# Optimization experiments

Hardware: AMD Instinct MI355X
Metric: run time of the kernel (lower is better)

## Reference

```python
import jax, jax.numpy as jnp
import numpy as np

N, E, F_IN, H, O = 50000, 800000, 128, 64, 1


def _gcn_conv(x, row, col, ew, W, b, n_nodes):
    """PyG GCNConv: add self-loops (weight 1), symmetric deg normalization,
    linear transform (no bias inside lin), scatter-add aggregation, then +bias."""
    loop = jnp.arange(n_nodes, dtype=row.dtype)
    r = jnp.concatenate([row, loop])
    c = jnp.concatenate([col, loop])
    w = jnp.concatenate([ew, jnp.ones((n_nodes,), dtype=ew.dtype)])
    deg = jax.ops.segment_sum(w, c, num_segments=n_nodes)            # [N]
    dis = jnp.where(deg > 0, jax.lax.rsqrt(jnp.maximum(deg, 1e-12)), 0.0)
    norm = dis[r] * w * dis[c]                                       # [E+N]
    h = x @ W                                                        # [N, out]
    msg = h[r] * norm[:, None]                                       # gather + scale
    agg = jax.ops.segment_sum(msg, c, num_segments=n_nodes)          # scatter-add
    return agg + b


def setup_inputs() -> dict:
    key = jax.random.key(0)
    ks = jax.random.split(key, 14)
    s = 0.02
    return {
        "x": jax.random.normal(ks[0], (N, F_IN), dtype=jnp.float32),
        "edge_index": jax.random.randint(ks[1], (2, E), 0, N, dtype=jnp.int64),
        "edge_weight": jax.random.uniform(ks[2], (E,), dtype=jnp.float32),
        "W1": jax.random.normal(ks[3], (F_IN, H), dtype=jnp.float32) * s,
        "b1": jnp.zeros((H,), dtype=jnp.float32),
        "W2": jax.random.normal(ks[4], (H, H), dtype=jnp.float32) * s,
        "b2": jnp.zeros((H,), dtype=jnp.float32),
        "W_ih": jax.random.normal(ks[5], (4 * H, H), dtype=jnp.float32) * s,
        "W_hh": jax.random.normal(ks[6], (4 * H, H), dtype=jnp.float32) * s,
        "b_ih": jax.random.normal(ks[7], (4 * H,), dtype=jnp.float32) * s,
        "b_hh": jax.random.normal(ks[8], (4 * H,), dtype=jnp.float32) * s,
        "W_reg": jax.random.normal(ks[9], (H, O), dtype=jnp.float32) * s,
        "b_reg": jnp.zeros((O,), dtype=jnp.float32),
    }


def reference(x, edge_index, edge_weight, W1, b1, W2, b2,
              W_ih, W_hh, b_ih, b_hh, W_reg, b_reg):
    row, col = edge_index[0], edge_index[1]
    n = x.shape[0]
    h = jax.nn.relu(_gcn_conv(x, row, col, edge_weight, W1, b1, n))
    h = jax.nn.relu(_gcn_conv(h, row, col, edge_weight, W2, b2, n))
    # single-step LSTM, zero initial (h0, c0); PyTorch gate order i, f, g, o
    hd = W_ih.shape[1]
    h0 = jnp.zeros((n, hd), dtype=h.dtype)
    gates = h @ W_ih.T + h0 @ W_hh.T + b_ih + b_hh                   # [N, 4H]
    i, f, g, o = jnp.split(gates, 4, axis=-1)
    c = jax.nn.sigmoid(f) * 0.0 + jax.nn.sigmoid(i) * jnp.tanh(g)    # c0 = 0
    hn = jax.nn.sigmoid(o) * jnp.tanh(c)                             # lstm_out[:, -1]
    return hn @ W_reg + b_reg
```

## Files before the change

### kernel.cpp

```cpp
#include <hip/hip_runtime.h>
#include <math.h>


#define QN 12544
#define NPAD (4 * QN)
#define NSLICE 64

__device__ __forceinline__ float sigmoidf_(float x) {
    return 1.0f / (1.0f + expf(-x));
}

__global__ __launch_bounds__(256) void hist_k(const int* __restrict__ col,
                                              int* __restrict__ part, int E, int N) {
    __shared__ int hloc[QN];
    const int t = threadIdx.x;
    const int s = blockIdx.x >> 2;
    const int q = blockIdx.x & 3;
    const int lo = q * QN;
    for (int i = t; i < QN; i += 256) hloc[i] = 0;
    __syncthreads();
    const int per = (E + NSLICE - 1) / NSLICE;
    const int e0 = s * per, e1 = min(E, e0 + per);
    for (int e = e0 + t; e < e1; e += 256) {
        int c = col[e];
        unsigned rel = (unsigned)(c - lo);
        if (rel < (unsigned)QN && (unsigned)c < (unsigned)N)
            atomicAdd(&hloc[rel], 1);
    }
    __syncthreads();
    int* dst = part + (size_t)s * NPAD + lo;
    for (int i = t; i < QN; i += 256) dst[i] = hloc[i];
}

__global__ __launch_bounds__(256) void hreduce_k(const int* __restrict__ part,
                                                 int* __restrict__ cnt) {
    int i = blockIdx.x * 256 + threadIdx.x;
    if (i >= NPAD) return;
    const int* p = part + i;
    int s0 = 0, s1 = 0, s2 = 0, s3 = 0;
    for (int s = 0; s < NSLICE; s += 4) {
        s0 += p[(size_t)(s + 0) * NPAD];
        s1 += p[(size_t)(s + 1) * NPAD];
        s2 += p[(size_t)(s + 2) * NPAD];
        s3 += p[(size_t)(s + 3) * NPAD];
    }
    cnt[i] = (s0 + s1) + (s2 + s3);
}

__global__ __launch_bounds__(256) void scanA_k(const int* __restrict__ cnt,
                                               int* __restrict__ bsum, int N) {
    __shared__ int r[256];
    int t = threadIdx.x, i = blockIdx.x * 256 + t;
    r[t] = (i < N) ? cnt[i] : 0;
    __syncthreads();
#pragma unroll
    for (int off = 128; off > 0; off >>= 1) {
        if (t < off) r[t] += r[t + off];
        __syncthreads();
    }
    if (t == 0) bsum[blockIdx.x] = r[0];
}

__global__ __launch_bounds__(256) void scanB_k(int* __restrict__ bsum,
                                               int* __restrict__ rowptr, int NB, int N) {
    __shared__ int s[2][256];
    int t = threadIdx.x;
    int v = (t < NB) ? bsum[t] : 0;
    int pin = 0;
    s[0][t] = v;
    __syncthreads();
#pragma unroll
    for (int off = 1; off < 256; off <<= 1) {
        int x = s[pin][t];
        if (t >= off) x += s[pin][t - off];
        s[pin ^ 1][t] = x;
        pin ^= 1;
        __syncthreads();
    }
    int incl = s[pin][t];
    if (t < NB) bsum[t] = incl - v;
    if (t == 255) rowptr[N] = incl;
}

__global__ __launch_bounds__(256) void scanC_k(const int* __restrict__ cnt,
                                               const int* __restrict__ bsum,
                                               int* __restrict__ rowptr,
                                               int* __restrict__ cursor, int N) {
    __shared__ int s[2][256];
    int t = threadIdx.x, i = blockIdx.x * 256 + t;
    int v = (i < N) ? cnt[i] : 0;
    int pin = 0;
    s[0][t] = v;
    __syncthreads();
#pragma unroll
    for (int off = 1; off < 256; off <<= 1) {
        int x = s[pin][t];
        if (t >= off) x += s[pin][t - off];
        s[pin ^ 1][t] = x;
        pin ^= 1;
        __syncthreads();
    }
    int excl = s[pin][t] - v + bsum[blockIdx.x];
    if (i < N) { rowptr[i] = excl; cursor[i] = excl; }
}

__global__ __launch_bounds__(256) void fill_k(const int* __restrict__ row,
                                              const int* __restrict__ col,
                                              const float* __restrict__ ew,
                                              int* __restrict__ cursor,
                                              int2* __restrict__ pairs, int E, int N) {
    int e = blockIdx.x * 256 + threadIdx.x;
    if (e >= E) return;
    int r = row[e], c = col[e];
    if ((unsigned)c >= (unsigned)N) return;
    float w = ew[e];
    if ((unsigned)r >= (unsigned)N) { r = 0; w = 0.0f; }
    int pos = __hip_atomic_fetch_add(&cursor[c], 1, __ATOMIC_RELAXED, __HIP_MEMORY_SCOPE_AGENT);
    pairs[pos] = make_int2(r, __float_as_int(w));
}

__global__ __launch_bounds__(256) void degsum_k(const int* __restrict__ rowptr,
                                                const int2* __restrict__ pairs,
                                                float* __restrict__ dis, int N) {
    int i = blockIdx.x * 256 + threadIdx.x;
    if (i >= N) return;
    int b = rowptr[i], en = rowptr[i + 1];
    float s = 0.0f;
    for (int e = b; e < en; ++e) s += __int_as_float(pairs[e].y);
    dis[i] = rsqrtf(s + 1.0f);
}

__global__ __launch_bounds__(256) void scale_k(int2* __restrict__ pairs,
                                               const float* __restrict__ dis, int E) {
    int e = blockIdx.x * 256 + threadIdx.x;
    if (e >= E) return;
    int2 p = pairs[e];
    p.y = __float_as_int(__int_as_float(p.y) * dis[p.x]);
    pairs[e] = p;
}

__global__ __launch_bounds__(256) void aggregate_k(const float* __restrict__ h,
                                                   const int* __restrict__ rowptr,
                                                   const int2* __restrict__ pairs,
                                                   const float* __restrict__ dis,
                                                   const float* __restrict__ b,
                                                   float* __restrict__ out, int N) {
    const int t = threadIdx.x;
    const int lane = t & 63;
    const int node = blockIdx.x * 4 + (t >> 6);
    if (node >= N) return;

    const int beg = rowptr[node], end = rowptr[node + 1];
    float acc = 0.0f;
    for (int base = beg; base < end; base += 64) {
        int n = min(64, end - base);
        int src = 0; float val = 0.0f;
        if (lane < n) {
            int2 p = pairs[base + lane];
            src = p.x; val = __int_as_float(p.y);
        }
        int j = 0;
        for (; j + 4 <= n; j += 4) {
            int   s0 = __shfl(src, j),     s1 = __shfl(src, j + 1);
            int   s2 = __shfl(src, j + 2), s3 = __shfl(src, j + 3);
            float v0 = __shfl(val, j),     v1 = __shfl(val, j + 1);
            float v2 = __shfl(val, j + 2), v3 = __shfl(val, j + 3);
            float h0 = h[(size_t)s0 * 64 + lane];
            float h1 = h[(size_t)s1 * 64 + lane];
            float h2 = h[(size_t)s2 * 64 + lane];
            float h3 = h[(size_t)s3 * 64 + lane];
            acc = fmaf(h0, v0, acc);
            acc = fmaf(h1, v1, acc);
            acc = fmaf(h2, v2, acc);
            acc = fmaf(h3, v3, acc);
        }
        for (; j < n; ++j) {
            int s0 = __shfl(src, j);
            float v0 = __shfl(val, j);
            acc = fmaf(h[(size_t)s0 * 64 + lane], v0, acc);
        }
    }
    float d = dis[node];
    acc = fmaf(d, h[(size_t)node * 64 + lane], acc);
    acc = fmaf(d, acc, b[lane]);
    out[(size_t)node * 64 + lane] = fmaxf(acc, 0.0f);
}

template <int K>
__global__ __launch_bounds__(256) void gemm64_k(const float* __restrict__ A,
                                                const float* __restrict__ W,
                                                float* __restrict__ C, int M) {
    __shared__ float xs[64][68];
    __shared__ float ws[K][64];
    const int t  = threadIdx.x;
    const int n0 = blockIdx.x * 64;

    for (int base = t * 4; base < K * 64; base += 1024)
        *(float4*)((float*)ws + base) = *(const float4*)(W + base);

    const int cg = t & 15, ng = t >> 4;
    const int col = cg * 4, nb = ng * 4;
    float acc[4][4];
#pragma unroll
    for (int i = 0; i < 4; ++i)
#pragma unroll
        for (int j = 0; j < 4; ++j) acc[i][j] = 0.0f;

    for (int k0 = 0; k0 < K; k0 += 64) {
        __syncthreads();
        for (int base = t * 4; base < 64 * 64; base += 1024) {
            int r = base >> 6, k = base & 63;
            int node = n0 + r;
            float4 v = make_float4(0.f, 0.f, 0.f, 0.f);
            if (node < M) v = *(const float4*)(A + (size_t)node * K + k0 + k);
            *(float4*)&xs[r][k] = v;
        }
        __syncthreads();
#pragma unroll 4
        for (int kk = 0; kk < 64; kk += 4) {
            float4 a[4];
#pragma unroll
            for (int i = 0; i < 4; ++i) a[i] = *(float4*)&xs[nb + i][kk];
#pragma unroll
            for (int j = 0; j < 4; ++j) {
                float4 bv = *(float4*)&ws[k0 + kk + j][col];
                float av[4];
                switch (j) {
                    case 0: av[0]=a[0].x; av[1]=a[1].x; av[2]=a[2].x; av[3]=a[3].x; break;
                    case 1: av[0]=a[0].y; av[1]=a[1].y; av[2]=a[2].y; av[3]=a[3].y; break;
                    case 2: av[0]=a[0].z; av[1]=a[1].z; av[2]=a[2].z; av[3]=a[3].z; break;
                    default:av[0]=a[0].w; av[1]=a[1].w; av[2]=a[2].w; av[3]=a[3].w; break;
                }
#pragma unroll
                for (int i = 0; i < 4; ++i) {
                    acc[i][0] = fmaf(av[i], bv.x, acc[i][0]);
                    acc[i][1] = fmaf(av[i], bv.y, acc[i][1]);
                    acc[i][2] = fmaf(av[i], bv.z, acc[i][2]);
                    acc[i][3] = fmaf(av[i], bv.w, acc[i][3]);
                }
            }
        }
    }
#pragma unroll
    for (int i = 0; i < 4; ++i) {
        int node = n0 + nb + i;
        if (node < M)
            *(float4*)(C + (size_t)node * 64 + col) =
                make_float4(acc[i][0], acc[i][1], acc[i][2], acc[i][3]);
    }
}

__global__ __launch_bounds__(256) void lstm_head_k(const float* __restrict__ h,
                                                   const float* __restrict__ Wih,
                                                   const float* __restrict__ bih,
                                                   const float* __restrict__ bhh,
                                                   const float* __restrict__ Wreg,
                                                   const float* __restrict__ breg,
                                                   float* __restrict__ out, int N) {
    __shared__ float wt[64 * 192];
    __shared__ float hsT[64 * 64];
    const int t = threadIdx.x;
    const int n0 = blockIdx.x * 64;

    {
        const int j = t & 63, kq = (t >> 6) * 4;
#pragma unroll
        for (int gid = 0; gid < 3; ++gid) {
            const int gBase = (gid == 0) ? 0 : (gid == 1 ? 128 : 192);
            const int gOff = gid * 64;
#pragma unroll
            for (int it = 0; it < 4; ++it) {
                int k0 = it * 16 + kq;
                float4 w = *(const float4*)(Wih + (size_t)(gBase + j) * 64 + k0);
                wt[(k0 + 0) * 192 + gOff + j] = w.x;
                wt[(k0 + 1) * 192 + gOff + j] = w.y;
                wt[(k0 + 2) * 192 + gOff + j] = w.z;
                wt[(k0 + 3) * 192 + gOff + j] = w.w;
            }
        }
    }
    {
        const int r = t & 63, kq = (t >> 6) * 4;
        const int node = n0 + r;
#pragma unroll
        for (int it = 0; it < 4; ++it) {
            int k0 = it * 16 + kq;
            float4 v = make_float4(0.f, 0.f, 0.f, 0.f);
            if (node < N) v = *(const float4*)(h + (size_t)node * 64 + k0);
            hsT[(k0 + 0) * 64 + r] = v.x;
            hsT[(k0 + 1) * 64 + r] = v.y;
            hsT[(k0 + 2) * 64 + r] = v.z;
            hsT[(k0 + 3) * 64 + r] = v.w;
        }
    }

    const int cg = t & 15, ng = t >> 4;
    const int col = cg * 4, nb = ng * 4;
    float4 bi4 = *(const float4*)(bih + col);
    float4 bg4 = *(const float4*)(bih + 128 + col);
    float4 bo4 = *(const float4*)(bih + 192 + col);
    {
        float4 h0 = *(const float4*)(bhh + col);
        float4 h1 = *(const float4*)(bhh + 128 + col);
        float4 h2 = *(const float4*)(bhh + 192 + col);
        bi4.x += h0.x; bi4.y += h0.y; bi4.z += h0.z; bi4.w += h0.w;
        bg4.x += h1.x; bg4.y += h1.y; bg4.z += h1.z; bg4.w += h1.w;
        bo4.x += h2.x; bo4.y += h2.y; bo4.z += h2.z; bo4.w += h2.w;
    }
    float4 wr4 = *(const float4*)(Wreg + col);
    const float br = breg[0];

    __syncthreads();

    float ai[4][4], ag[4][4], ao[4][4];
#pragma unroll
    for (int i = 0; i < 4; ++i)
#pragma unroll
        for (int j = 0; j < 4; ++j) { ai[i][j] = 0.f; ag[i][j] = 0.f; ao[i][j] = 0.f; }

#pragma unroll 4
    for (int k = 0; k < 64; ++k) {
        float4 a  = *(float4*)&hsT[k * 64 + nb];
        float4 wi = *(float4*)&wt[k * 192 + col];
        float4 wg = *(float4*)&wt[k * 192 + 64 + col];
        float4 wo = *(float4*)&wt[k * 192 + 128 + col];
        const float av[4] = {a.x, a.y, a.z, a.w};
#pragma unroll
        for (int i = 0; i < 4; ++i) {
            ai[i][0] = fmaf(av[i], wi.x, ai[i][0]);
            ai[i][1] = fmaf(av[i], wi.y, ai[i][1]);
            ai[i][2] = fmaf(av[i], wi.z, ai[i][2]);
            ai[i][3] = fmaf(av[i], wi.w, ai[i][3]);
            ag[i][0] = fmaf(av[i], wg.x, ag[i][0]);
            ag[i][1] = fmaf(av[i], wg.y, ag[i][1]);
            ag[i][2] = fmaf(av[i], wg.z, ag[i][2]);
            ag[i][3] = fmaf(av[i], wg.w, ag[i][3]);
            ao[i][0] = fmaf(av[i], wo.x, ao[i][0]);
            ao[i][1] = fmaf(av[i], wo.y, ao[i][1]);
            ao[i][2] = fmaf(av[i], wo.z, ao[i][2]);
            ao[i][3] = fmaf(av[i], wo.w, ao[i][3]);
        }
    }

    const float bia[4] = {bi4.x, bi4.y, bi4.z, bi4.w};
    const float bga[4] = {bg4.x, bg4.y, bg4.z, bg4.w};
    const float boa[4] = {bo4.x, bo4.y, bo4.z, bo4.w};
    const float wra[4] = {wr4.x, wr4.y, wr4.z, wr4.w};
    float res[4];
#pragma unroll
    for (int i = 0; i < 4; ++i) {
        float s = 0.f;
#pragma unroll
        for (int j = 0; j < 4; ++j) {
            float gi = ai[i][j] + bia[j];
            float gg = ag[i][j] + bga[j];
            float go = ao[i][j] + boa[j];
            float cc = sigmoidf_(gi) * tanhf(gg);
            float hn = sigmoidf_(go) * tanhf(cc);
            s = fmaf(hn, wra[j], s);
        }
        res[i] = s;
    }
#pragma unroll
    for (int off = 8; off > 0; off >>= 1) {
#pragma unroll
        for (int i = 0; i < 4; ++i) res[i] += __shfl_down(res[i], off);
    }
    if (cg == 0) {
#pragma unroll
        for (int i = 0; i < 4; ++i) {
            int node = n0 + nb + i;
            if (node < N) out[node] = res[i] + br;
        }
    }
}

extern "C" void kernel_launch(void* const* d_in, const int* in_sizes, int n_in,
                              void* d_out, int out_size, void* d_ws, size_t ws_size,
                              hipStream_t stream) {
    const float* x    = (const float*)d_in[0];
    const int*   ei   = (const int*)d_in[1];
    const float* ew   = (const float*)d_in[2];
    const float* W1   = (const float*)d_in[3];
    const float* b1   = (const float*)d_in[4];
    const float* W2   = (const float*)d_in[5];
    const float* b2   = (const float*)d_in[6];
    const float* Wih  = (const float*)d_in[7];
    const float* bih  = (const float*)d_in[9];
    const float* bhh  = (const float*)d_in[10];
    const float* Wreg = (const float*)d_in[11];
    const float* breg = (const float*)d_in[12];
    float* out = (float*)d_out;

    const int N = out_size;
    const int E = in_sizes[1] / 2;
    const int* row = ei;
    const int* col = ei + E;

    const int NB = (N + 255) / 256;

    char* wsb = (char*)d_ws;
    size_t off = 0;
    int*   part   = (int*)  (wsb + off);
    float* bufA   = (float*)(wsb + off); off += (size_t)NSLICE * NPAD * 4;
    int2*  pairs  = (int2*) (wsb + off); off += (size_t)E * 8;
    float* dis    = (float*)(wsb + off); off += (size_t)NPAD * 4;
    int*   cnt    = (int*)  (wsb + off); off += (size_t)NPAD * 4;
    int*   rowptr = (int*)  (wsb + off); off += ((size_t)NPAD + 64) * 4;
    int*   cursor = (int*)  (wsb + off); off += (size_t)NPAD * 4;
    int*   bsum   = (int*)  (wsb + off); off += 1024;
    float* bufB   = (float*)(wsb + off); off += (size_t)N * 64 * 4;
    float* bufC   = (float*)(wsb + off); off += (size_t)N * 64 * 4;

    const int eb = (E + 255) / 256;
    const int gb = (N + 63) / 64;
    const int ab = (N + 3) / 4;

    hist_k<<<NSLICE * 4, 256, 0, stream>>>(col, part, E, N);
    hreduce_k<<<NPAD / 256, 256, 0, stream>>>(part, cnt);
    scanA_k<<<NB, 256, 0, stream>>>(cnt, bsum, N);
    scanB_k<<<1, 256, 0, stream>>>(bsum, rowptr, NB, N);
    scanC_k<<<NB, 256, 0, stream>>>(cnt, bsum, rowptr, cursor, N);
    fill_k<<<eb, 256, 0, stream>>>(row, col, ew, cursor, pairs, E, N);
    degsum_k<<<NB, 256, 0, stream>>>(rowptr, pairs, dis, N);
    scale_k<<<eb, 256, 0, stream>>>(pairs, dis, E);

    gemm64_k<128><<<gb, 256, 0, stream>>>(x, W1, bufA, N);
    aggregate_k<<<ab, 256, 0, stream>>>(bufA, rowptr, pairs, dis, b1, bufB, N);

    gemm64_k<64><<<gb, 256, 0, stream>>>(bufB, W2, bufC, N);
    aggregate_k<<<ab, 256, 0, stream>>>(bufC, rowptr, pairs, dis, b2, bufA, N);

    lstm_head_k<<<gb, 256, 0, stream>>>(bufA, Wih, bih, bhh, Wreg, breg, out, N);
}
```

Baseline: 313.8 us.

## Compute degree in histogram and fill CSR via per-slice LDS cursors with full norm

The histogram pass now also accumulates edge weights per slice, so the per-slice prefix kernel produces slice offsets, counts and inverse-sqrt degrees together. Filling then uses per-slice shared-memory cursors instead of global atomics, and stores the fully normalized weight (w*dis[r]*dis[c]). This removes the separate degree-sum and scale kernels and the contended global atomics. In exchange it adds a second float histogram in LDS (doubling shared memory per block and lowering occupancy), writes the slice offset array, and has fill re-scan all edges over 256 blocks. The aggregate epilogue is adjusted to apply the self-loop term as d*d.

```diff
diff --git a/kernel.cpp b/kernel.cpp
--- a/kernel.cpp
+++ b/kernel.cpp
@@ -11,40 +11,48 @@
 }
 
 __global__ __launch_bounds__(256) void hist_k(const int* __restrict__ col,
-                                              int* __restrict__ part, int E, int N) {
-    __shared__ int hloc[QN];
+                                              const float* __restrict__ ew,
+                                              int* __restrict__ part_i,
+                                              float* __restrict__ part_f, int E, int N) {
+    __shared__ int   hc[QN];
+    __shared__ float hw[QN];
     const int t = threadIdx.x;
     const int s = blockIdx.x >> 2;
     const int q = blockIdx.x & 3;
     const int lo = q * QN;
-    for (int i = t; i < QN; i += 256) hloc[i] = 0;
+    for (int i = t; i < QN; i += 256) { hc[i] = 0; hw[i] = 0.0f; }
     __syncthreads();
     const int per = (E + NSLICE - 1) / NSLICE;
     const int e0 = s * per, e1 = min(E, e0 + per);
     for (int e = e0 + t; e < e1; e += 256) {
         int c = col[e];
         unsigned rel = (unsigned)(c - lo);
-        if (rel < (unsigned)QN && (unsigned)c < (unsigned)N)
-            atomicAdd(&hloc[rel], 1);
-    }
-    __syncthreads();
-    int* dst = part + (size_t)s * NPAD + lo;
-    for (int i = t; i < QN; i += 256) dst[i] = hloc[i];
-}
-
-__global__ __launch_bounds__(256) void hreduce_k(const int* __restrict__ part,
-                                                 int* __restrict__ cnt) {
+        if (rel < (unsigned)QN && (unsigned)c < (unsigned)N) {
+            atomicAdd(&hc[rel], 1);
+            atomicAdd(&hw[rel], ew[e]);
+        }
+    }
+    __syncthreads();
+    int*   di = part_i + (size_t)s * NPAD + lo;
+    float* df = part_f + (size_t)s * NPAD + lo;
+    for (int i = t; i < QN; i += 256) { di[i] = hc[i]; df[i] = hw[i]; }
+}
+
+__global__ __launch_bounds__(256) void prefix_k(const int* __restrict__ part_i,
+                                                const float* __restrict__ part_f,
+                                                int* __restrict__ coff,
+                                                int* __restrict__ cnt,
+                                                float* __restrict__ dis) {
     int i = blockIdx.x * 256 + threadIdx.x;
-    if (i >= NPAD) return;
-    const int* p = part + i;
-    int s0 = 0, s1 = 0, s2 = 0, s3 = 0;
-    for (int s = 0; s < NSLICE; s += 4) {
-        s0 += p[(size_t)(s + 0) * NPAD];
-        s1 += p[(size_t)(s + 1) * NPAD];
-        s2 += p[(size_t)(s + 2) * NPAD];
-        s3 += p[(size_t)(s + 3) * NPAD];
-    }
-    cnt[i] = (s0 + s1) + (s2 + s3);
+    int acc = 0; float wacc = 0.0f;
+    for (int s = 0; s < NSLICE; ++s) {
+        size_t idx = (size_t)s * NPAD + i;
+        coff[idx] = acc;
+        acc  += part_i[idx];
+        wacc += part_f[idx];
+    }
+    cnt[i] = acc;
+    dis[i] = rsqrtf(wacc + 1.0f);
 }
 
 __global__ __launch_bounds__(256) void scanA_k(const int* __restrict__ cnt,
@@ -84,8 +92,7 @@
 
 __global__ __launch_bounds__(256) void scanC_k(const int* __restrict__ cnt,
                                                const int* __restrict__ bsum,
-                                               int* __restrict__ rowptr,
-                                               int* __restrict__ cursor, int N) {
+                                               int* __restrict__ rowptr, int N) {
     __shared__ int s[2][256];
     int t = threadIdx.x, i = blockIdx.x * 256 + t;
     int v = (i < N) ? cnt[i] : 0;
@@ -101,42 +108,39 @@
         __syncthreads();
     }
     int excl = s[pin][t] - v + bsum[blockIdx.x];
-    if (i < N) { rowptr[i] = excl; cursor[i] = excl; }
+    if (i < N) rowptr[i] = excl;
 }
 
 __global__ __launch_bounds__(256) void fill_k(const int* __restrict__ row,
                                               const int* __restrict__ col,
                                               const float* __restrict__ ew,
-                                              int* __restrict__ cursor,
+                                              const int* __restrict__ rowptr,
+                                              const int* __restrict__ coff,
+                                              const float* __restrict__ dis,
                                               int2* __restrict__ pairs, int E, int N) {
-    int e = blockIdx.x * 256 + threadIdx.x;
-    if (e >= E) return;
-    int r = row[e], c = col[e];
-    if ((unsigned)c >= (unsigned)N) return;
-    float w = ew[e];
-    if ((unsigned)r >= (unsigned)N) { r = 0; w = 0.0f; }
-    int pos = __hip_atomic_fetch_add(&cursor[c], 1, __ATOMIC_RELAXED, __HIP_MEMORY_SCOPE_AGENT);
-    pairs[pos] = make_int2(r, __float_as_int(w));
-}
-
-__global__ __launch_bounds__(256) void degsum_k(const int* __restrict__ rowptr,
-                                                const int2* __restrict__ pairs,
-                                                float* __restrict__ dis, int N) {
-    int i = blockIdx.x * 256 + threadIdx.x;
-    if (i >= N) return;
-    int b = rowptr[i], en = rowptr[i + 1];
-    float s = 0.0f;
-    for (int e = b; e < en; ++e) s += __int_as_float(pairs[e].y);
-    dis[i] = rsqrtf(s + 1.0f);
-}
-
-__global__ __launch_bounds__(256) void scale_k(int2* __restrict__ pairs,
-                                               const float* __restrict__ dis, int E) {
-    int e = blockIdx.x * 256 + threadIdx.x;
-    if (e >= E) return;
-    int2 p = pairs[e];
-    p.y = __float_as_int(__int_as_float(p.y) * dis[p.x]);
-    pairs[e] = p;
+    __shared__ int lcur[QN];
+    const int t = threadIdx.x;
+    const int s = blockIdx.x >> 2;
+    const int q = blockIdx.x & 3;
+    const int lo = q * QN;
+    const int* cof = coff + (size_t)s * NPAD + lo;
+    const int* rp  = rowptr + lo;
+    for (int i = t; i < QN; i += 256) lcur[i] = rp[i] + cof[i];
+    __syncthreads();
+    const int per = (E + NSLICE - 1) / NSLICE;
+    const int e0 = s * per, e1 = min(E, e0 + per);
+    for (int e = e0 + t; e < e1; e += 256) {
+        int c = col[e];
+        unsigned rel = (unsigned)(c - lo);
+        if (rel < (unsigned)QN && (unsigned)c < (unsigned)N) {
+            int r = row[e];
+            float w = ew[e];
+            if ((unsigned)r >= (unsigned)N) { r = 0; w = 0.0f; }
+            float nv = w * dis[r] * dis[c];
+            int pos = atomicAdd(&lcur[rel], 1);
+            pairs[pos] = make_int2(r, __float_as_int(nv));
+        }
+    }
 }
 
 __global__ __launch_bounds__(256) void aggregate_k(const float* __restrict__ h,
@@ -181,8 +185,7 @@
         }
     }
     float d = dis[node];
-    acc = fmaf(d, h[(size_t)node * 64 + lane], acc);
-    acc = fmaf(d, acc, b[lane]);
+    acc = fmaf(d * d, h[(size_t)node * 64 + lane], acc) + b[lane];
     out[(size_t)node * 64 + lane] = fmaxf(acc, 0.0f);
 }
 
@@ -399,31 +402,31 @@
 
     const int NB = (N + 255) / 256;
 
+    const size_t REG = ((size_t)NSLICE * NPAD > (size_t)N * 64 ? (size_t)NSLICE * NPAD
+                                                               : (size_t)N * 64) * 4;
     char* wsb = (char*)d_ws;
     size_t off = 0;
-    int*   part   = (int*)  (wsb + off);
-    float* bufA   = (float*)(wsb + off); off += (size_t)NSLICE * NPAD * 4;
+    int*   part_i = (int*)  (wsb + off);
+    float* bufA   = (float*)(wsb + off); off += REG;
+    float* part_f = (float*)(wsb + off);
+    float* bufB   = (float*)(wsb + off); off += REG;
+    int*   coff   = (int*)  (wsb + off);
+    float* bufC   = (float*)(wsb + off); off += REG;
     int2*  pairs  = (int2*) (wsb + off); off += (size_t)E * 8;
     float* dis    = (float*)(wsb + off); off += (size_t)NPAD * 4;
     int*   cnt    = (int*)  (wsb + off); off += (size_t)NPAD * 4;
     int*   rowptr = (int*)  (wsb + off); off += ((size_t)NPAD + 64) * 4;
-    int*   cursor = (int*)  (wsb + off); off += (size_t)NPAD * 4;
     int*   bsum   = (int*)  (wsb + off); off += 1024;
-    float* bufB   = (float*)(wsb + off); off += (size_t)N * 64 * 4;
-    float* bufC   = (float*)(wsb + off); off += (size_t)N * 64 * 4;
-
-    const int eb = (E + 255) / 256;
+
     const int gb = (N + 63) / 64;
     const int ab = (N + 3) / 4;
 
-    hist_k<<<NSLICE * 4, 256, 0, stream>>>(col, part, E, N);
-    hreduce_k<<<NPAD / 256, 256, 0, stream>>>(part, cnt);
+    hist_k<<<NSLICE * 4, 256, 0, stream>>>(col, ew, part_i, part_f, E, N);
+    prefix_k<<<NPAD / 256, 256, 0, stream>>>(part_i, part_f, coff, cnt, dis);
     scanA_k<<<NB, 256, 0, stream>>>(cnt, bsum, N);
     scanB_k<<<1, 256, 0, stream>>>(bsum, rowptr, NB, N);
-    scanC_k<<<NB, 256, 0, stream>>>(cnt, bsum, rowptr, cursor, N);
-    fill_k<<<eb, 256, 0, stream>>>(row, col, ew, cursor, pairs, E, N);
-    degsum_k<<<NB, 256, 0, stream>>>(rowptr, pairs, dis, N);
-    scale_k<<<eb, 256, 0, stream>>>(pairs, dis, E);
+    scanC_k<<<NB, 256, 0, stream>>>(cnt, bsum, rowptr, N);
+    fill_k<<<NSLICE * 4, 256, 0, stream>>>(row, col, ew, rowptr, coff, dis, pairs, E, N);
 
     gemm64_k<128><<<gb, 256, 0, stream>>>(x, W1, bufA, N);
     aggregate_k<<<ab, 256, 0, stream>>>(bufA, rowptr, pairs, dis, b1, bufB, N);
```

After: 311.2 us. Within noise of the previous version (-0.8%).

## Replace global-atomic CSR fill with slice-local LDS cursors; aggregate two nodes per wave

Applied to the files above, without the earlier changes.

Histogram now uses 128 edge slices times 8 node octants with 16-bit per-slice counts. A prefix kernel turns these into per-slice offsets, so the fill kernel can place edges using LDS atomics on per-slice cursors instead of global atomics on a cursor array. The aggregate kernel processes two destination nodes per wavefront so more gathers are in flight at once. Workspace regions are overlapped to fit the new 16-bit buffers. The 16-bit counts would overflow if one slice put more than 65535 edges on a single node, and each fill block rescans its whole edge slice for every octant.

```diff
diff --git a/kernel.cpp b/kernel.cpp
--- a/kernel.cpp
+++ b/kernel.cpp
@@ -2,49 +2,58 @@
 #include <math.h>
 
 
-#define QN 12544
-#define NPAD (4 * QN)
-#define NSLICE 64
+#define QN 6272
+#define NOCT 8
+#define NPAD (NOCT * QN)
+#define NSLICE 128
 
 __device__ __forceinline__ float sigmoidf_(float x) {
     return 1.0f / (1.0f + expf(-x));
 }
 
 __global__ __launch_bounds__(256) void hist_k(const int* __restrict__ col,
-                                              int* __restrict__ part, int E, int N) {
-    __shared__ int hloc[QN];
+                                              unsigned short* __restrict__ part,
+                                              int E, int N) {
+    __shared__ int hc[QN];
     const int t = threadIdx.x;
-    const int s = blockIdx.x >> 2;
-    const int q = blockIdx.x & 3;
+    const int s = blockIdx.x >> 3;
+    const int q = blockIdx.x & 7;
     const int lo = q * QN;
-    for (int i = t; i < QN; i += 256) hloc[i] = 0;
+    for (int i = t; i < QN; i += 256) hc[i] = 0;
     __syncthreads();
     const int per = (E + NSLICE - 1) / NSLICE;
     const int e0 = s * per, e1 = min(E, e0 + per);
-    for (int e = e0 + t; e < e1; e += 256) {
+    int e = e0 + t;
+    for (; e + 768 < e1; e += 1024) {
+        int c0 = col[e], c1 = col[e + 256], c2 = col[e + 512], c3 = col[e + 768];
+        unsigned r0 = (unsigned)(c0 - lo), r1 = (unsigned)(c1 - lo);
+        unsigned r2 = (unsigned)(c2 - lo), r3 = (unsigned)(c3 - lo);
+        if (r0 < (unsigned)QN && (unsigned)c0 < (unsigned)N) atomicAdd(&hc[r0], 1);
+        if (r1 < (unsigned)QN && (unsigned)c1 < (unsigned)N) atomicAdd(&hc[r1], 1);
+        if (r2 < (unsigned)QN && (unsigned)c2 < (unsigned)N) atomicAdd(&hc[r2], 1);
+        if (r3 < (unsigned)QN && (unsigned)c3 < (unsigned)N) atomicAdd(&hc[r3], 1);
+    }
+    for (; e < e1; e += 256) {
         int c = col[e];
         unsigned rel = (unsigned)(c - lo);
-        if (rel < (unsigned)QN && (unsigned)c < (unsigned)N)
-            atomicAdd(&hloc[rel], 1);
-    }
-    __syncthreads();
-    int* dst = part + (size_t)s * NPAD + lo;
-    for (int i = t; i < QN; i += 256) dst[i] = hloc[i];
-}
-
-__global__ __launch_bounds__(256) void hreduce_k(const int* __restrict__ part,
-                                                 int* __restrict__ cnt) {
+        if (rel < (unsigned)QN && (unsigned)c < (unsigned)N) atomicAdd(&hc[rel], 1);
+    }
+    __syncthreads();
+    unsigned short* dst = part + (size_t)s * NPAD + lo;
+    for (int i = t; i < QN; i += 256) dst[i] = (unsigned short)hc[i];
+}
+
+__global__ __launch_bounds__(256) void prefix_k(const unsigned short* __restrict__ part,
+                                                unsigned short* __restrict__ coff,
+                                                int* __restrict__ cnt) {
     int i = blockIdx.x * 256 + threadIdx.x;
-    if (i >= NPAD) return;
-    const int* p = part + i;
-    int s0 = 0, s1 = 0, s2 = 0, s3 = 0;
-    for (int s = 0; s < NSLICE; s += 4) {
-        s0 += p[(size_t)(s + 0) * NPAD];
-        s1 += p[(size_t)(s + 1) * NPAD];
-        s2 += p[(size_t)(s + 2) * NPAD];
-        s3 += p[(size_t)(s + 3) * NPAD];
-    }
-    cnt[i] = (s0 + s1) + (s2 + s3);
+    int acc = 0;
+    for (int s = 0; s < NSLICE; ++s) {
+        size_t idx = (size_t)s * NPAD + i;
+        coff[idx] = (unsigned short)acc;
+        acc += part[idx];
+    }
+    cnt[i] = acc;
 }
 
 __global__ __launch_bounds__(256) void scanA_k(const int* __restrict__ cnt,
@@ -84,8 +93,7 @@
 
 __global__ __launch_bounds__(256) void scanC_k(const int* __restrict__ cnt,
                                                const int* __restrict__ bsum,
-                                               int* __restrict__ rowptr,
-                                               int* __restrict__ cursor, int N) {
+                                               int* __restrict__ rowptr, int N) {
     __shared__ int s[2][256];
     int t = threadIdx.x, i = blockIdx.x * 256 + t;
     int v = (i < N) ? cnt[i] : 0;
@@ -101,22 +109,61 @@
         __syncthreads();
     }
     int excl = s[pin][t] - v + bsum[blockIdx.x];
-    if (i < N) { rowptr[i] = excl; cursor[i] = excl; }
+    if (i < N) rowptr[i] = excl;
 }
 
 __global__ __launch_bounds__(256) void fill_k(const int* __restrict__ row,
                                               const int* __restrict__ col,
                                               const float* __restrict__ ew,
-                                              int* __restrict__ cursor,
+                                              const int* __restrict__ rowptr,
+                                              const unsigned short* __restrict__ coff,
                                               int2* __restrict__ pairs, int E, int N) {
-    int e = blockIdx.x * 256 + threadIdx.x;
-    if (e >= E) return;
-    int r = row[e], c = col[e];
-    if ((unsigned)c >= (unsigned)N) return;
-    float w = ew[e];
-    if ((unsigned)r >= (unsigned)N) { r = 0; w = 0.0f; }
-    int pos = __hip_atomic_fetch_add(&cursor[c], 1, __ATOMIC_RELAXED, __HIP_MEMORY_SCOPE_AGENT);
-    pairs[pos] = make_int2(r, __float_as_int(w));
+    __shared__ int lcur[QN];
+    const int t = threadIdx.x;
+    const int s = blockIdx.x >> 3;
+    const int q = blockIdx.x & 7;
+    const int lo = q * QN;
+    const unsigned short* cof = coff + (size_t)s * NPAD + lo;
+    const int* rp = rowptr + lo;
+    for (int i = t; i < QN; i += 256) lcur[i] = rp[i] + (int)cof[i];
+    __syncthreads();
+    const int per = (E + NSLICE - 1) / NSLICE;
+    const int e0 = s * per, e1 = min(E, e0 + per);
+    int e = e0 + t;
+    for (; e + 768 < e1; e += 1024) {
+        int c0 = col[e], c1 = col[e + 256], c2 = col[e + 512], c3 = col[e + 768];
+        unsigned r0 = (unsigned)(c0 - lo), r1 = (unsigned)(c1 - lo);
+        unsigned r2 = (unsigned)(c2 - lo), r3 = (unsigned)(c3 - lo);
+        if (r0 < (unsigned)QN && (unsigned)c0 < (unsigned)N) {
+            int r = row[e]; float w = ew[e];
+            if ((unsigned)r >= (unsigned)N) { r = 0; w = 0.0f; }
+            pairs[atomicAdd(&lcur[r0], 1)] = make_int2(r, __float_as_int(w));
+        }
+        if (r1 < (unsigned)QN && (unsigned)c1 < (unsigned)N) {
+            int r = row[e + 256]; float w = ew[e + 256];
+            if ((unsigned)r >= (unsigned)N) { r = 0; w = 0.0f; }
+            pairs[atomicAdd(&lcur[r1], 1)] = make_int2(r, __float_as_int(w));
+        }
+        if (r2 < (unsigned)QN && (unsigned)c2 < (unsigned)N) {
+            int r = row[e + 512]; float w = ew[e + 512];
+            if ((unsigned)r >= (unsigned)N) { r = 0; w = 0.0f; }
+            pairs[atomicAdd(&lcur[r2], 1)] = make_int2(r, __float_as_int(w));
+        }
+        if (r3 < (unsigned)QN && (unsigned)c3 < (unsigned)N) {
+            int r = row[e + 768]; float w = ew[e + 768];
+            if ((unsigned)r >= (unsigned)N) { r = 0; w = 0.0f; }
+            pairs[atomicAdd(&lcur[r3], 1)] = make_int2(r, __float_as_int(w));
+        }
+    }
+    for (; e < e1; e += 256) {
+        int c = col[e];
+        unsigned rel = (unsigned)(c - lo);
+        if (rel < (unsigned)QN && (unsigned)c < (unsigned)N) {
+            int r = row[e]; float w = ew[e];
+            if ((unsigned)r >= (unsigned)N) { r = 0; w = 0.0f; }
+            pairs[atomicAdd(&lcur[rel], 1)] = make_int2(r, __float_as_int(w));
+        }
+    }
 }
 
 __global__ __launch_bounds__(256) void degsum_k(const int* __restrict__ rowptr,
@@ -147,43 +194,73 @@
                                                    float* __restrict__ out, int N) {
     const int t = threadIdx.x;
     const int lane = t & 63;
-    const int node = blockIdx.x * 4 + (t >> 6);
-    if (node >= N) return;
-
-    const int beg = rowptr[node], end = rowptr[node + 1];
-    float acc = 0.0f;
-    for (int base = beg; base < end; base += 64) {
-        int n = min(64, end - base);
-        int src = 0; float val = 0.0f;
-        if (lane < n) {
-            int2 p = pairs[base + lane];
-            src = p.x; val = __int_as_float(p.y);
-        }
+    const int n0 = (blockIdx.x * 4 + (t >> 6)) * 2;
+    if (n0 >= N) return;
+    const int n1 = n0 + 1;
+
+    const int beg0 = rowptr[n0];
+    const int end0 = rowptr[n0 + 1];
+    const int beg1 = end0;
+    const int end1 = (n1 < N) ? rowptr[n1 + 1] : end0;
+    const int len0 = end0 - beg0, len1 = end1 - beg1;
+    const int L = max(len0, len1);
+
+    float acc0 = 0.0f, acc1 = 0.0f;
+    for (int base = 0; base < L; base += 64) {
+        const int m0 = min(64, len0 - base);
+        const int m1 = min(64, len1 - base);
+        int s0r = 0, s1r = 0; float v0r = 0.0f, v1r = 0.0f;
+        if (lane < m0) {
+            int2 p = pairs[beg0 + base + lane];
+            s0r = p.x; v0r = __int_as_float(p.y);
+        }
+        if (lane < m1) {
+            int2 p = pairs[beg1 + base + lane];
+            s1r = p.x; v1r = __int_as_float(p.y);
+        }
+        const int m = max(m0, m1);
         int j = 0;
-        for (; j + 4 <= n; j += 4) {
-            int   s0 = __shfl(src, j),     s1 = __shfl(src, j + 1);
-            int   s2 = __shfl(src, j + 2), s3 = __shfl(src, j + 3);
-            float v0 = __shfl(val, j),     v1 = __shfl(val, j + 1);
-            float v2 = __shfl(val, j + 2), v3 = __shfl(val, j + 3);
-            float h0 = h[(size_t)s0 * 64 + lane];
-            float h1 = h[(size_t)s1 * 64 + lane];
-            float h2 = h[(size_t)s2 * 64 + lane];
-            float h3 = h[(size_t)s3 * 64 + lane];
-            acc = fmaf(h0, v0, acc);
-            acc = fmaf(h1, v1, acc);
-            acc = fmaf(h2, v2, acc);
-            acc = fmaf(h3, v3, acc);
-        }
-        for (; j < n; ++j) {
-            int s0 = __shfl(src, j);
-            float v0 = __shfl(val, j);
-            acc = fmaf(h[(size_t)s0 * 64 + lane], v0, acc);
-        }
-    }
-    float d = dis[node];
-    acc = fmaf(d, h[(size_t)node * 64 + lane], acc);
-    acc = fmaf(d, acc, b[lane]);
-    out[(size_t)node * 64 + lane] = fmaxf(acc, 0.0f);
+        for (; j + 4 <= m; j += 4) {
+            int   a0 = __shfl(s0r, j),     a1 = __shfl(s0r, j + 1);
+            int   a2 = __shfl(s0r, j + 2), a3 = __shfl(s0r, j + 3);
+            int   b0 = __shfl(s1r, j),     b1 = __shfl(s1r, j + 1);
+            int   b2 = __shfl(s1r, j + 2), b3 = __shfl(s1r, j + 3);
+            float x0 = __shfl(v0r, j),     x1 = __shfl(v0r, j + 1);
+            float x2 = __shfl(v0r, j + 2), x3 = __shfl(v0r, j + 3);
+            float y0 = __shfl(v1r, j),     y1 = __shfl(v1r, j + 1);
+            float y2 = __shfl(v1r, j + 2), y3 = __shfl(v1r, j + 3);
+            float ha0 = h[(size_t)a0 * 64 + lane];
+            float ha1 = h[(size_t)a1 * 64 + lane];
+            float ha2 = h[(size_t)a2 * 64 + lane];
+            float ha3 = h[(size_t)a3 * 64 + lane];
+            float hb0 = h[(size_t)b0 * 64 + lane];
+            float hb1 = h[(size_t)b1 * 64 + lane];
+            float hb2 = h[(size_t)b2 * 64 + lane];
+            float hb3 = h[(size_t)b3 * 64 + lane];
+            acc0 = fmaf(ha0, x0, acc0); acc0 = fmaf(ha1, x1, acc0);
+            acc0 = fmaf(ha2, x2, acc0); acc0 = fmaf(ha3, x3, acc0);
+            acc1 = fmaf(hb0, y0, acc1); acc1 = fmaf(hb1, y1, acc1);
+            acc1 = fmaf(hb2, y2, acc1); acc1 = fmaf(hb3, y3, acc1);
+        }
+        for (; j < m; ++j) {
+            int   a0 = __shfl(s0r, j), b0 = __shfl(s1r, j);
+            float x0 = __shfl(v0r, j), y0 = __shfl(v1r, j);
+            acc0 = fmaf(h[(size_t)a0 * 64 + lane], x0, acc0);
+            acc1 = fmaf(h[(size_t)b0 * 64 + lane], y0, acc1);
+        }
+    }
+    {
+        float d = dis[n0];
+        acc0 = fmaf(d, h[(size_t)n0 * 64 + lane], acc0);
+        acc0 = fmaf(d, acc0, b[lane]);
+        out[(size_t)n0 * 64 + lane] = fmaxf(acc0, 0.0f);
+    }
+    if (n1 < N) {
+        float d = dis[n1];
+        acc1 = fmaf(d, h[(size_t)n1 * 64 + lane], acc1);
+        acc1 = fmaf(d, acc1, b[lane]);
+        out[(size_t)n1 * 64 + lane] = fmaxf(acc1, 0.0f);
+    }
 }
 
 template <int K>
@@ -398,30 +475,34 @@
     const int* col = ei + E;
 
     const int NB = (N + 255) / 256;
+    const int eb = (E + 255) / 256;
+
+    const size_t R16 = (size_t)NSLICE * NPAD * 2;
+    const size_t RF  = (size_t)N * 64 * 4;
+    const size_t REG = (R16 > RF ? R16 : RF + 255) & ~(size_t)255;
 
     char* wsb = (char*)d_ws;
     size_t off = 0;
-    int*   part   = (int*)  (wsb + off);
-    float* bufA   = (float*)(wsb + off); off += (size_t)NSLICE * NPAD * 4;
+    unsigned short* part = (unsigned short*)(wsb + off);
+    float*          bufA = (float*)(wsb + off); off += REG;
+    unsigned short* coff = (unsigned short*)(wsb + off);
+    float*          bufC = (float*)(wsb + off); off += REG;
+    float*          bufB = (float*)(wsb + off); off += REG;
     int2*  pairs  = (int2*) (wsb + off); off += (size_t)E * 8;
     float* dis    = (float*)(wsb + off); off += (size_t)NPAD * 4;
     int*   cnt    = (int*)  (wsb + off); off += (size_t)NPAD * 4;
     int*   rowptr = (int*)  (wsb + off); off += ((size_t)NPAD + 64) * 4;
-    int*   cursor = (int*)  (wsb + off); off += (size_t)NPAD * 4;
     int*   bsum   = (int*)  (wsb + off); off += 1024;
-    float* bufB   = (float*)(wsb + off); off += (size_t)N * 64 * 4;
-    float* bufC   = (float*)(wsb + off); off += (size_t)N * 64 * 4;
-
-    const int eb = (E + 255) / 256;
+
     const int gb = (N + 63) / 64;
-    const int ab = (N + 3) / 4;
-
-    hist_k<<<NSLICE * 4, 256, 0, stream>>>(col, part, E, N);
-    hreduce_k<<<NPAD / 256, 256, 0, stream>>>(part, cnt);
+    const int ab = (N + 7) / 8;
+
+    hist_k<<<NSLICE * NOCT, 256, 0, stream>>>(col, part, E, N);
+    prefix_k<<<NPAD / 256, 256, 0, stream>>>(part, coff, cnt);
     scanA_k<<<NB, 256, 0, stream>>>(cnt, bsum, N);
     scanB_k<<<1, 256, 0, stream>>>(bsum, rowptr, NB, N);
-    scanC_k<<<NB, 256, 0, stream>>>(cnt, bsum, rowptr, cursor, N);
-    fill_k<<<eb, 256, 0, stream>>>(row, col, ew, cursor, pairs, E, N);
+    scanC_k<<<NB, 256, 0, stream>>>(cnt, bsum, rowptr, N);
+    fill_k<<<NSLICE * NOCT, 256, 0, stream>>>(row, col, ew, rowptr, coff, pairs, E, N);
     degsum_k<<<NB, 256, 0, stream>>>(rowptr, pairs, dis, N);
     scale_k<<<eb, 256, 0, stream>>>(pairs, dis, E);
 
```

Measured after the change: 280.3 us. -10.7%, faster.
